# Kernel optimization log

Measured on AMD Instinct MI355X. Metric: run time of the kernel, lower is better.

The kernel has to match this reference:

```python
import jax, jax.numpy as jnp
import numpy as np

N = 200000   # nodes
E = 6400000  # edges
F = 128      # input node features
H = 6        # hiddenSize (module constant)
C = 10       # num_classes
G = 64       # graphs in batch


def setup_inputs() -> dict:
    key = jax.random.key(0)
    ks = jax.random.split(key, 7)
    x = jax.random.normal(ks[0], (N, F), dtype=jnp.float32)
    edge_index = jax.random.randint(ks[1], (2, E), 0, N, dtype=jnp.int32)
    batch = jnp.sort(jax.random.randint(ks[2], (N,), 0, G, dtype=jnp.int32))
    W1 = jax.random.normal(ks[3], (F, H), dtype=jnp.float32) * (1.0 / np.sqrt(F))
    b1 = jnp.zeros((H,), dtype=jnp.float32)
    W2 = jax.random.normal(ks[4], (H, C), dtype=jnp.float32) * (1.0 / np.sqrt(H))
    b2 = jnp.zeros((C,), dtype=jnp.float32)
    return {"x": x, "edge_index": edge_index, "batch": batch,
            "W1": W1, "b1": b1, "W2": W2, "b2": b2}


def _gcn_conv(x, W, b, row, col, dis):
    # PyG GCNConv: h = x W; out = D^{-1/2}(A+I)D^{-1/2} h + b
    h = x @ W                                      # [N, out]
    norm = dis[row] * dis[col]                     # [E] edge normalization
    msg = norm[:, None] * h[row]                   # gather from source nodes
    agg = jax.ops.segment_sum(msg, col, num_segments=N)  # scatter-add to targets
    # self-loop term: norm = dis[i]*dis[i]
    return agg + (dis * dis)[:, None] * h + b


def reference(x, edge_index, batch, W1, b1, W2, b2):
    row, col = edge_index[0], edge_index[1]
    # degree after adding self-loops (edge_weight = 1)
    deg = jax.ops.segment_sum(jnp.ones((E,), dtype=x.dtype), col, num_segments=N) + 1.0
    dis = jax.lax.rsqrt(deg)                       # deg^{-1/2}

    h = _gcn_conv(x, W1, b1, row, col, dis)
    h = jax.nn.relu(h)
    # dropout is identity in inference mode
    h = _gcn_conv(h, W2, b2, row, col, dis)        # [N, C]

    # global mean pool over each graph
    sums = jax.ops.segment_sum(h, batch, num_segments=G)                  # [G, C]
    cnts = jax.ops.segment_sum(jnp.ones((N,), dtype=h.dtype), batch, num_segments=G)
    pooled = sums / jnp.maximum(cnts, 1.0)[:, None]
    return jax.nn.log_softmax(pooled, axis=1)      # [G, C]
```

## Files before the change

### kernel.cpp

```cpp
#include <hip/hip_runtime.h>
#include <math.h>

#define N_NODES 200000
#define N_EDGES 6400000
#define F_IN    128
#define H_HID   6
#define C_OUT   10
#define G_BATCH 64

#define TILE_E  8192
#define NT      ((N_EDGES + TILE_E - 1) / TILE_E)
#define EPT     (TILE_E / 512)
#define BSH     9
#define BNODES  512
#define NBUCK   ((N_NODES + BNODES - 1) / BNODES)
#define BCAP    18432
#define QCAP    10240

__device__ __forceinline__ unsigned short f2bf(float f) {
    unsigned u = __float_as_uint(f);
    u += 0x7fff + ((u >> 16) & 1);
    return (unsigned short)(u >> 16);
}
__device__ __forceinline__ unsigned pack2(float a, float b) {
    return (unsigned)f2bf(a) | ((unsigned)f2bf(b) << 16);
}
__device__ __forceinline__ float bf_lo(unsigned u) { return __uint_as_float(u << 16); }
__device__ __forceinline__ float bf_hi(unsigned u) { return __uint_as_float(u & 0xffff0000u); }

__global__ __launch_bounds__(512) void scatterA_kernel(const int* __restrict__ row,
                                                       const int* __restrict__ col,
                                                       int* __restrict__ gcur,
                                                       int* __restrict__ binned, int E) {
    __shared__ int sortbuf[TILE_E];
    __shared__ int cnt[512];
    __shared__ int pos[513];
    __shared__ int lbase[512];
    int t = blockIdx.x, tid = threadIdx.x;
    int base = t * TILE_E;
    int tile_n = min(TILE_E, E - base);

    cnt[tid] = 0;
    __syncthreads();

    int myval[EPT];
#pragma unroll
    for (int k = 0; k < EPT; ++k) {
        int e = base + k * 512 + tid;
        if (e < E) {
            int c = col[e];
            myval[k] = ((c & (BNODES - 1)) << 18) | row[e];
            atomicAdd(&cnt[c >> BSH], 1);
        }
    }
    __syncthreads();

    pos[tid] = cnt[tid];
    __syncthreads();
    for (int off = 1; off < 512; off <<= 1) {
        int tv = (tid >= off) ? pos[tid - off] : 0;
        __syncthreads();
        pos[tid] += tv;
        __syncthreads();
    }
    int incl = pos[tid];
    __syncthreads();
    {
        int c = cnt[tid];
        int excl = incl - c;
        pos[tid] = excl;
        cnt[tid] = excl;
        if (tid == 511) pos[512] = incl;
        if (tid < NBUCK) {
            lbase[tid] = tid * BCAP + (c ? atomicAdd(&gcur[tid], c) : 0);
        }
    }
    __syncthreads();

#pragma unroll
    for (int k = 0; k < EPT; ++k) {
        int e = base + k * 512 + tid;
        if (e < E) {
            int b = col[e] >> BSH;
            int p = atomicAdd(&cnt[b], 1);
            sortbuf[p] = myval[k];
        }
    }
    __syncthreads();

    for (int i = tid; i < tile_n; i += 512) {
        int lo = 0, hi = NBUCK - 1;
        while (lo < hi) {
            int mid = (lo + hi + 1) >> 1;
            if (pos[mid] <= i) lo = mid; else hi = mid - 1;
        }
        binned[lbase[lo] + (i - pos[lo])] = sortbuf[i];
    }
}

__global__ __launch_bounds__(1024) void passB_kernel(const int* __restrict__ gcur,
                                                     const int* __restrict__ binned,
                                                     int* __restrict__ offs, int* __restrict__ endo,
                                                     float* __restrict__ dis,
                                                     int* __restrict__ csr, int E) {
    __shared__ int cnt[512];
    __shared__ int scn[512];
    __shared__ int cur[256];
    __shared__ int sortbuf[QCAP];
    int b = blockIdx.x, tid = threadIdx.x;
    int bb = b * BCAP;
    int be = bb + gcur[b];
    if (tid < 512) cnt[tid] = 0;
    __syncthreads();
    int e = bb + tid;
    for (; e + 3072 < be; e += 4096) {
        int p0 = binned[e], p1 = binned[e + 1024], p2 = binned[e + 2048], p3 = binned[e + 3072];
        atomicAdd(&cnt[p0 >> 18], 1); atomicAdd(&cnt[p1 >> 18], 1);
        atomicAdd(&cnt[p2 >> 18], 1); atomicAdd(&cnt[p3 >> 18], 1);
    }
    for (; e < be; e += 1024) atomicAdd(&cnt[binned[e] >> 18], 1);
    __syncthreads();
    int v = (tid < 512) ? cnt[tid] : 0;
    if (tid < 512) scn[tid] = v;
    __syncthreads();
    for (int off = 1; off < 512; off <<= 1) {
        int t2 = (tid < 512 && tid >= off) ? scn[tid - off] : 0;
        __syncthreads();
        if (tid < 512) scn[tid] += t2;
        __syncthreads();
    }
    if (tid < 512) {
        int excl = scn[tid] - v;
        scn[tid] = excl;
        int n = (b << BSH) + tid;
        if (n < N_NODES) {
            offs[n] = bb + excl;
            endo[n] = bb + excl + v;
            dis[n] = rsqrtf((float)v + 1.0f);
        }
    }
    __syncthreads();
    int total = be - bb;
#define PLACE(p) { int loc = (p) >> 18; if ((loc >> 8) == q) {                      \
        int ps = scn[loc] - qbase + atomicAdd(&cur[loc & 255], 1);                  \
        if (ps < QCAP) sortbuf[ps] = (p) & 0x3FFFF;                                 \
        else csr[bb + qbase + ps] = (p) & 0x3FFFF; } }
    for (int q = 0; q < 2; ++q) {
        int qbase = scn[q << 8];
        int qend = (q == 0) ? scn[256] : total;
        int qn = qend - qbase;
        if (tid < 256) cur[tid] = 0;
        __syncthreads();
        int e2 = bb + tid;
        for (; e2 + 3072 < be; e2 += 4096) {
            int p0 = binned[e2], p1 = binned[e2 + 1024], p2 = binned[e2 + 2048], p3 = binned[e2 + 3072];
            PLACE(p0) PLACE(p1) PLACE(p2) PLACE(p3)
        }
        for (; e2 < be; e2 += 1024) { int p = binned[e2]; PLACE(p) }
        __syncthreads();
        int lim = qn < QCAP ? qn : QCAP;
        for (int i = tid; i < lim; i += 1024) csr[bb + qbase + i] = sortbuf[i];
        __syncthreads();
    }
#undef PLACE
}

__global__ void xw1_kernel(const float* __restrict__ x, const float* __restrict__ W1,
                           const float* __restrict__ dis, uint4* __restrict__ h1b) {
    __shared__ float w[F_IN * H_HID];
    for (int i = threadIdx.x; i < F_IN * H_HID; i += blockDim.x) w[i] = W1[i];
    __syncthreads();
    int n = blockIdx.x * blockDim.x + threadIdx.x;
    if (n >= N_NODES) return;
    float acc[H_HID] = {0.f, 0.f, 0.f, 0.f, 0.f, 0.f};
    const float4* xr = (const float4*)(x + (size_t)n * F_IN);
#pragma unroll 4
    for (int f4 = 0; f4 < F_IN / 4; ++f4) {
        float4 v = xr[f4];
        int f = f4 * 4;
#pragma unroll
        for (int j = 0; j < H_HID; ++j) {
            acc[j] += v.x * w[(f + 0) * H_HID + j] + v.y * w[(f + 1) * H_HID + j]
                    + v.z * w[(f + 2) * H_HID + j] + v.w * w[(f + 3) * H_HID + j];
        }
    }
    float d = dis[n];
    uint4 o;
    o.x = pack2(d * acc[0], d * acc[1]);
    o.y = pack2(d * acc[2], d * acc[3]);
    o.z = pack2(d * acc[4], d * acc[5]);
    o.w = __float_as_uint(d);
    h1b[n] = o;
}

__global__ void gather1_kernel(const int* __restrict__ offs, const int* __restrict__ endo,
                               const int* __restrict__ csr,
                               const uint4* __restrict__ h1b, const float* __restrict__ b1,
                               uint4* __restrict__ rs) {
    int grp = threadIdx.x >> 3, sub = threadIdx.x & 7;
    int n = blockIdx.x * 32 + grp;
    int s = offs[n], e_end = endo[n];
    float a[H_HID] = {0.f, 0.f, 0.f, 0.f, 0.f, 0.f};
    int e = s + sub;
    for (; e + 24 < e_end; e += 32) {
        int i0 = csr[e], i1 = csr[e + 8], i2 = csr[e + 16], i3 = csr[e + 24];
        uint4 v0 = h1b[i0], v1 = h1b[i1], v2 = h1b[i2], v3 = h1b[i3];
        a[0] += (bf_lo(v0.x) + bf_lo(v1.x)) + (bf_lo(v2.x) + bf_lo(v3.x));
        a[1] += (bf_hi(v0.x) + bf_hi(v1.x)) + (bf_hi(v2.x) + bf_hi(v3.x));
        a[2] += (bf_lo(v0.y) + bf_lo(v1.y)) + (bf_lo(v2.y) + bf_lo(v3.y));
        a[3] += (bf_hi(v0.y) + bf_hi(v1.y)) + (bf_hi(v2.y) + bf_hi(v3.y));
        a[4] += (bf_lo(v0.z) + bf_lo(v1.z)) + (bf_lo(v2.z) + bf_lo(v3.z));
        a[5] += (bf_hi(v0.z) + bf_hi(v1.z)) + (bf_hi(v2.z) + bf_hi(v3.z));
    }
    for (; e < e_end; e += 8) {
        uint4 v = h1b[csr[e]];
        a[0] += bf_lo(v.x); a[1] += bf_hi(v.x);
        a[2] += bf_lo(v.y); a[3] += bf_hi(v.y);
        a[4] += bf_lo(v.z); a[5] += bf_hi(v.z);
    }
#pragma unroll
    for (int j = 0; j < H_HID; ++j)
#pragma unroll
        for (int off = 4; off > 0; off >>= 1) a[j] += __shfl_xor(a[j], off);
    uint4 self = h1b[n];
    float d = __uint_as_float(self.w);
    float sf[H_HID] = {bf_lo(self.x), bf_hi(self.x), bf_lo(self.y),
                       bf_hi(self.y), bf_lo(self.z), bf_hi(self.z)};
    if (sub == 0) {
        float r[H_HID];
#pragma unroll
        for (int j = 0; j < H_HID; ++j) {
            float vv = d * (a[j] + sf[j]) + b1[j];
            r[j] = d * (vv > 0.f ? vv : 0.f);
        }
        uint4 o;
        o.x = pack2(r[0], r[1]);
        o.y = pack2(r[2], r[3]);
        o.z = pack2(r[4], r[5]);
        o.w = self.w;
        rs[n] = o;
    }
}

__global__ void gather2_pool_kernel(const int* __restrict__ offs, const int* __restrict__ endo,
                                    const int* __restrict__ csr,
                                    const uint4* __restrict__ rs, const float* __restrict__ W2,
                                    const int* __restrict__ batch, float* __restrict__ sums) {
    __shared__ float w2s[H_HID * C_OUT];
    __shared__ float nodeval[32][C_OUT];
    __shared__ int lg[32];
    if (threadIdx.x < H_HID * C_OUT) w2s[threadIdx.x] = W2[threadIdx.x];
    __syncthreads();
    int grp = threadIdx.x >> 3, sub = threadIdx.x & 7;
    int n = blockIdx.x * 32 + grp;
    int s = offs[n], e_end = endo[n];
    float a[H_HID] = {0.f, 0.f, 0.f, 0.f, 0.f, 0.f};
    int e = s + sub;
    for (; e + 24 < e_end; e += 32) {
        int i0 = csr[e], i1 = csr[e + 8], i2 = csr[e + 16], i3 = csr[e + 24];
        uint4 v0 = rs[i0], v1 = rs[i1], v2 = rs[i2], v3 = rs[i3];
        a[0] += (bf_lo(v0.x) + bf_lo(v1.x)) + (bf_lo(v2.x) + bf_lo(v3.x));
        a[1] += (bf_hi(v0.x) + bf_hi(v1.x)) + (bf_hi(v2.x) + bf_hi(v3.x));
        a[2] += (bf_lo(v0.y) + bf_lo(v1.y)) + (bf_lo(v2.y) + bf_lo(v3.y));
        a[3] += (bf_hi(v0.y) + bf_hi(v1.y)) + (bf_hi(v2.y) + bf_hi(v3.y));
        a[4] += (bf_lo(v0.z) + bf_lo(v1.z)) + (bf_lo(v2.z) + bf_lo(v3.z));
        a[5] += (bf_hi(v0.z) + bf_hi(v1.z)) + (bf_hi(v2.z) + bf_hi(v3.z));
    }
    for (; e < e_end; e += 8) {
        uint4 v = rs[csr[e]];
        a[0] += bf_lo(v.x); a[1] += bf_hi(v.x);
        a[2] += bf_lo(v.y); a[3] += bf_hi(v.y);
        a[4] += bf_lo(v.z); a[5] += bf_hi(v.z);
    }
#pragma unroll
    for (int j = 0; j < H_HID; ++j)
#pragma unroll
        for (int off = 4; off > 0; off >>= 1) a[j] += __shfl_xor(a[j], off);
    uint4 self = rs[n];
    float d = __uint_as_float(self.w);
    float t[H_HID] = {a[0] + bf_lo(self.x), a[1] + bf_hi(self.x), a[2] + bf_lo(self.y),
                      a[3] + bf_hi(self.y), a[4] + bf_lo(self.z), a[5] + bf_hi(self.z)};
    {
        float acc = 0.f;
#pragma unroll
        for (int j = 0; j < H_HID; ++j) acc += t[j] * w2s[j * C_OUT + sub];
        nodeval[grp][sub] = d * acc;
        if (sub < 2) {
            float acc2 = 0.f;
#pragma unroll
            for (int j = 0; j < H_HID; ++j) acc2 += t[j] * w2s[j * C_OUT + sub + 8];
            nodeval[grp][sub + 8] = d * acc2;
        }
    }
    if (sub == 0) lg[grp] = batch[n];
    __syncthreads();
    if (threadIdx.x < C_OUT) {
        int c = threadIdx.x;
        float acc = 0.f;
        int gcur2 = lg[0];
#pragma unroll
        for (int w = 0; w < 32; ++w) {
            if (lg[w] != gcur2) {
                atomicAdd(&sums[gcur2 * C_OUT + c], acc);
                gcur2 = lg[w]; acc = 0.f;
            }
            acc += nodeval[w][c];
        }
        atomicAdd(&sums[gcur2 * C_OUT + c], acc);
    }
}

__global__ void pool_finish_kernel(const float* __restrict__ sums, const int* __restrict__ batch,
                                   const float* __restrict__ b2, float* __restrict__ out) {
    int g = threadIdx.x;
    if (g >= G_BATCH) return;
    int lo = 0, hi = N_NODES;
    while (lo < hi) { int mid = (lo + hi) >> 1; if (batch[mid] < g) lo = mid + 1; else hi = mid; }
    int c0 = lo;
    hi = N_NODES;
    while (lo < hi) { int mid = (lo + hi) >> 1; if (batch[mid] < g + 1) lo = mid + 1; else hi = mid; }
    float inv = 1.0f / fmaxf((float)(lo - c0), 1.0f);
    float v[C_OUT], m = -INFINITY;
#pragma unroll
    for (int c = 0; c < C_OUT; ++c) {
        v[c] = sums[g * C_OUT + c] * inv + b2[c];
        m = fmaxf(m, v[c]);
    }
    float s = 0.f;
#pragma unroll
    for (int c = 0; c < C_OUT; ++c) s += expf(v[c] - m);
    float lse = m + logf(s);
#pragma unroll
    for (int c = 0; c < C_OUT; ++c) out[g * C_OUT + c] = v[c] - lse;
}

extern "C" void kernel_launch(void* const* d_in, const int* in_sizes, int n_in,
                              void* d_out, int out_size, void* d_ws, size_t ws_size,
                              hipStream_t stream) {
    const float* x   = (const float*)d_in[0];
    const int* ei    = (const int*)d_in[1];
    const int* row   = ei;
    const int* col   = ei + N_EDGES;
    const int* batch = (const int*)d_in[2];
    const float* W1  = (const float*)d_in[3];
    const float* b1  = (const float*)d_in[4];
    const float* W2  = (const float*)d_in[5];
    const float* b2  = (const float*)d_in[6];
    float* out = (float*)d_out;

    char* p = (char*)d_ws;
    float* sums   = (float*)p;  p += (size_t)G_BATCH * C_OUT * 4;
    int*   gcur   = (int*)p;    p += (size_t)400 * 4;
    int*   offs   = (int*)p;    p += (size_t)N_NODES * 4;
    int*   endo   = (int*)p;    p += (size_t)N_NODES * 4;
    float* dis    = (float*)p;  p += (size_t)N_NODES * 4;
    int*   csr    = (int*)p;    p += (size_t)NBUCK * BCAP * 4;
    int*   binned = (int*)p;
    uint4* h1b    = (uint4*)binned;
    uint4* rs     = (uint4*)binned + N_NODES;

    hipMemsetAsync(sums, 0, (size_t)G_BATCH * C_OUT * 4 + 400 * 4, stream);

    scatterA_kernel<<<NT, 512, 0, stream>>>(row, col, gcur, binned, N_EDGES);
    passB_kernel   <<<NBUCK, 1024, 0, stream>>>(gcur, binned, offs, endo, dis, csr, N_EDGES);
    xw1_kernel     <<<(N_NODES + 255) / 256, 256, 0, stream>>>(x, W1, dis, h1b);
    gather1_kernel <<<N_NODES / 32, 256, 0, stream>>>(offs, endo, csr, h1b, b1, rs);
    gather2_pool_kernel<<<N_NODES / 32, 256, 0, stream>>>(offs, endo, csr, rs, W2, batch, sums);
    pool_finish_kernel <<<1, 64, 0, stream>>>(sums, batch, b2, out);
}
```

Before: 361.3 us.

## Use wave-shuffle scans, vectorized edge loads, and single-pass LDS bucket sort

The scatter kernel now gives each thread 16 contiguous edges read with int4 loads and keeps the bucket ids in registers, so col is not reloaded. The block prefix scans in both kernels change from log-step shared-memory loops with many barriers to wave shuffle scans plus a small cross-wave fix-up. passB now stages the whole bucket (up to BCAP ints, 72KB) in LDS and places every element in one pass, replacing two passes over binned with an overflow path. The larger LDS footprint limits how many passB blocks fit per CU, and the contiguous-per-thread layout changes the global access pattern.

```diff
diff --git a/kernel.cpp b/kernel.cpp
--- a/kernel.cpp
+++ b/kernel.cpp
@@ -10,12 +10,11 @@
 
 #define TILE_E  8192
 #define NT      ((N_EDGES + TILE_E - 1) / TILE_E)
-#define EPT     (TILE_E / 512)
+#define EPT     16
 #define BSH     9
 #define BNODES  512
 #define NBUCK   ((N_NODES + BNODES - 1) / BNODES)
 #define BCAP    18432
-#define QCAP    10240
 
 __device__ __forceinline__ unsigned short f2bf(float f) {
     unsigned u = __float_as_uint(f);
@@ -28,14 +27,15 @@
 __device__ __forceinline__ float bf_lo(unsigned u) { return __uint_as_float(u << 16); }
 __device__ __forceinline__ float bf_hi(unsigned u) { return __uint_as_float(u & 0xffff0000u); }
 
-__global__ __launch_bounds__(512) void scatterA_kernel(const int* __restrict__ row,
-                                                       const int* __restrict__ col,
-                                                       int* __restrict__ gcur,
-                                                       int* __restrict__ binned, int E) {
+__global__ __launch_bounds__(512, 8) void scatterA_kernel(const int* __restrict__ row,
+                                                          const int* __restrict__ col,
+                                                          int* __restrict__ gcur,
+                                                          int* __restrict__ binned, int E) {
     __shared__ int sortbuf[TILE_E];
     __shared__ int cnt[512];
     __shared__ int pos[513];
     __shared__ int lbase[512];
+    __shared__ int wtot[8];
     int t = blockIdx.x, tid = threadIdx.x;
     int base = t * TILE_E;
     int tile_n = min(TILE_E, E - base);
@@ -44,45 +44,69 @@
     __syncthreads();
 
     int myval[EPT];
+    int myb[EPT];
+    int ebase = base + tid * EPT;
+    if (ebase + EPT <= E) {
+        const int4* c4 = (const int4*)(col + ebase);
+        const int4* r4 = (const int4*)(row + ebase);
+#pragma unroll
+        for (int q = 0; q < EPT / 4; ++q) {
+            int4 c = c4[q];
+            int4 r = r4[q];
+            int k = q * 4;
+            myval[k + 0] = ((c.x & (BNODES - 1)) << 18) | r.x;  myb[k + 0] = c.x >> BSH;
+            myval[k + 1] = ((c.y & (BNODES - 1)) << 18) | r.y;  myb[k + 1] = c.y >> BSH;
+            myval[k + 2] = ((c.z & (BNODES - 1)) << 18) | r.z;  myb[k + 2] = c.z >> BSH;
+            myval[k + 3] = ((c.w & (BNODES - 1)) << 18) | r.w;  myb[k + 3] = c.w >> BSH;
+        }
+#pragma unroll
+        for (int k = 0; k < EPT; ++k) atomicAdd(&cnt[myb[k]], 1);
+    } else {
+#pragma unroll
+        for (int k = 0; k < EPT; ++k) {
+            int e = ebase + k;
+            if (e < E) {
+                int c = col[e];
+                myval[k] = ((c & (BNODES - 1)) << 18) | row[e];
+                myb[k] = c >> BSH;
+                atomicAdd(&cnt[myb[k]], 1);
+            } else {
+                myb[k] = -1;
+            }
+        }
+    }
+    __syncthreads();
+
+    int c = cnt[tid];
+    int v = c;
+    int lane = tid & 63, wid = tid >> 6;
+#pragma unroll
+    for (int off = 1; off < 64; off <<= 1) {
+        int u = __shfl_up(v, off);
+        if (lane >= off) v += u;
+    }
+    if (lane == 63) wtot[wid] = v;
+    __syncthreads();
+    if (tid == 0) {
+        int running = 0;
+#pragma unroll
+        for (int i = 0; i < 8; ++i) { int w = wtot[i]; wtot[i] = running; running += w; }
+    }
+    __syncthreads();
+    int incl = v + wtot[wid];
+    int excl = incl - c;
+    pos[tid] = excl;
+    cnt[tid] = excl;
+    if (tid == 511) pos[512] = incl;
+    if (tid < NBUCK) {
+        lbase[tid] = tid * BCAP + (c ? atomicAdd(&gcur[tid], c) : 0);
+    }
+    __syncthreads();
+
 #pragma unroll
     for (int k = 0; k < EPT; ++k) {
-        int e = base + k * 512 + tid;
-        if (e < E) {
-            int c = col[e];
-            myval[k] = ((c & (BNODES - 1)) << 18) | row[e];
-            atomicAdd(&cnt[c >> BSH], 1);
-        }
-    }
-    __syncthreads();
-
-    pos[tid] = cnt[tid];
-    __syncthreads();
-    for (int off = 1; off < 512; off <<= 1) {
-        int tv = (tid >= off) ? pos[tid - off] : 0;
-        __syncthreads();
-        pos[tid] += tv;
-        __syncthreads();
-    }
-    int incl = pos[tid];
-    __syncthreads();
-    {
-        int c = cnt[tid];
-        int excl = incl - c;
-        pos[tid] = excl;
-        cnt[tid] = excl;
-        if (tid == 511) pos[512] = incl;
-        if (tid < NBUCK) {
-            lbase[tid] = tid * BCAP + (c ? atomicAdd(&gcur[tid], c) : 0);
-        }
-    }
-    __syncthreads();
-
-#pragma unroll
-    for (int k = 0; k < EPT; ++k) {
-        int e = base + k * 512 + tid;
-        if (e < E) {
-            int b = col[e] >> BSH;
-            int p = atomicAdd(&cnt[b], 1);
+        if (myb[k] >= 0) {
+            int p = atomicAdd(&cnt[myb[k]], 1);
             sortbuf[p] = myval[k];
         }
     }
@@ -103,15 +127,16 @@
                                                      int* __restrict__ offs, int* __restrict__ endo,
                                                      float* __restrict__ dis,
                                                      int* __restrict__ csr, int E) {
+    __shared__ int stage[BCAP];
     __shared__ int cnt[512];
-    __shared__ int scn[512];
-    __shared__ int cur[256];
-    __shared__ int sortbuf[QCAP];
+    __shared__ int wtot[8];
     int b = blockIdx.x, tid = threadIdx.x;
     int bb = b * BCAP;
-    int be = bb + gcur[b];
+    int total = gcur[b];
+    int be = bb + total;
     if (tid < 512) cnt[tid] = 0;
     __syncthreads();
+
     int e = bb + tid;
     for (; e + 3072 < be; e += 4096) {
         int p0 = binned[e], p1 = binned[e + 1024], p2 = binned[e + 2048], p3 = binned[e + 3072];
@@ -120,49 +145,54 @@
     }
     for (; e < be; e += 1024) atomicAdd(&cnt[binned[e] >> 18], 1);
     __syncthreads();
-    int v = (tid < 512) ? cnt[tid] : 0;
-    if (tid < 512) scn[tid] = v;
-    __syncthreads();
-    for (int off = 1; off < 512; off <<= 1) {
-        int t2 = (tid < 512 && tid >= off) ? scn[tid - off] : 0;
+
+    if (tid < 512) {
+        int v0 = cnt[tid];
+        int v = v0;
+        int lane = tid & 63, wid = tid >> 6;
+#pragma unroll
+        for (int off = 1; off < 64; off <<= 1) {
+            int u = __shfl_up(v, off);
+            if (lane >= off) v += u;
+        }
+        if (lane == 63) wtot[wid] = v;
         __syncthreads();
-        if (tid < 512) scn[tid] += t2;
+        if (tid == 0) {
+            int running = 0;
+#pragma unroll
+            for (int i = 0; i < 8; ++i) { int w = wtot[i]; wtot[i] = running; running += w; }
+        }
         __syncthreads();
-    }
-    if (tid < 512) {
-        int excl = scn[tid] - v;
-        scn[tid] = excl;
+        int incl = v + wtot[wid];
+        int excl = incl - v0;
+        cnt[tid] = excl;
         int n = (b << BSH) + tid;
         if (n < N_NODES) {
             offs[n] = bb + excl;
-            endo[n] = bb + excl + v;
-            dis[n] = rsqrtf((float)v + 1.0f);
-        }
-    }
-    __syncthreads();
-    int total = be - bb;
-#define PLACE(p) { int loc = (p) >> 18; if ((loc >> 8) == q) {                      \
-        int ps = scn[loc] - qbase + atomicAdd(&cur[loc & 255], 1);                  \
-        if (ps < QCAP) sortbuf[ps] = (p) & 0x3FFFF;                                 \
-        else csr[bb + qbase + ps] = (p) & 0x3FFFF; } }
-    for (int q = 0; q < 2; ++q) {
-        int qbase = scn[q << 8];
-        int qend = (q == 0) ? scn[256] : total;
-        int qn = qend - qbase;
-        if (tid < 256) cur[tid] = 0;
+            endo[n] = bb + excl + v0;
+            dis[n] = rsqrtf((float)v0 + 1.0f);
+        }
+    } else {
         __syncthreads();
-        int e2 = bb + tid;
-        for (; e2 + 3072 < be; e2 += 4096) {
-            int p0 = binned[e2], p1 = binned[e2 + 1024], p2 = binned[e2 + 2048], p3 = binned[e2 + 3072];
-            PLACE(p0) PLACE(p1) PLACE(p2) PLACE(p3)
-        }
-        for (; e2 < be; e2 += 1024) { int p = binned[e2]; PLACE(p) }
         __syncthreads();
-        int lim = qn < QCAP ? qn : QCAP;
-        for (int i = tid; i < lim; i += 1024) csr[bb + qbase + i] = sortbuf[i];
-        __syncthreads();
-    }
-#undef PLACE
+    }
+    __syncthreads();
+
+    e = bb + tid;
+    for (; e + 3072 < be; e += 4096) {
+        int p0 = binned[e], p1 = binned[e + 1024], p2 = binned[e + 2048], p3 = binned[e + 3072];
+        int s0 = atomicAdd(&cnt[p0 >> 18], 1); stage[s0] = p0 & 0x3FFFF;
+        int s1 = atomicAdd(&cnt[p1 >> 18], 1); stage[s1] = p1 & 0x3FFFF;
+        int s2 = atomicAdd(&cnt[p2 >> 18], 1); stage[s2] = p2 & 0x3FFFF;
+        int s3 = atomicAdd(&cnt[p3 >> 18], 1); stage[s3] = p3 & 0x3FFFF;
+    }
+    for (; e < be; e += 1024) {
+        int p = binned[e];
+        int s = atomicAdd(&cnt[p >> 18], 1); stage[s] = p & 0x3FFFF;
+    }
+    __syncthreads();
+
+    for (int i = tid; i < total; i += 1024) csr[bb + i] = stage[i];
 }
 
 __global__ void xw1_kernel(const float* __restrict__ x, const float* __restrict__ W1,
```

Result: faster. 342.7 us (-5.1%).
